# Kernel optimization log

Hardware: AMD Instinct MI355X
Metric: run time of the kernel (lower is better)

The kernel has to match this reference:

```python
import jax, jax.numpy as jnp
import numpy as np

N_LEVELS = 16
N_FEAT = 2
LOG2_T = 19
T = 2 ** LOG2_T
BASE_RES = 2 ** 4
MAX_RES = 2 ** 11
PER_LEVEL_SCALE = np.exp((np.log(MAX_RES) - np.log(BASE_RES)) / (N_LEVELS - 1))
RESOLUTIONS = [int(np.floor(BASE_RES * PER_LEVEL_SCALE ** lv)) + 1 for lv in range(N_LEVELS)]
INIT_ACTIVE_LEVEL = 8
N_POINTS = 1048576
N_OUT = N_LEVELS * N_FEAT
# tcnn spatial hashing primes
P1 = jnp.uint32(2654435761)
P2 = jnp.uint32(805459861)


def _level_lookup(x, tbl, res):
    """x: [N,3] in [0,1], tbl: [T,F], res: python int grid resolution."""
    pos = x * (res - 1)                       # [N,3]
    c0 = jnp.clip(jnp.floor(pos).astype(jnp.int32), 0, res - 2)
    w = pos - c0.astype(pos.dtype)            # [N,3] trilinear fractions
    feats = jnp.zeros((x.shape[0], tbl.shape[-1]), dtype=tbl.dtype)
    dense = (res ** 3) <= T                   # static per level: dense grid vs hashed
    for dz in (0, 1):
        for dy in (0, 1):
            for dx in (0, 1):
                offs = jnp.array([dx, dy, dz], jnp.int32)
                c = c0 + offs                 # [N,3] corner int coords
                if dense:
                    idx = c[:, 0] + res * (c[:, 1] + res * c[:, 2])
                else:
                    cu = c.astype(jnp.uint32)
                    idx = ((cu[:, 0]) ^ (cu[:, 1] * P1) ^ (cu[:, 2] * P2)) & jnp.uint32(T - 1)
                    idx = idx.astype(jnp.int32)
                # trilinear corner weight: prod over axes of (w if offs==1 else 1-w)
                wc = jnp.prod(jnp.where(offs == 1, w, 1.0 - w), axis=-1)  # [N]
                feats = feats + tbl[idx] * wc[:, None]
    return feats


def setup_inputs() -> dict:
    key = jax.random.key(0)
    k1, k2 = jax.random.split(key)
    x = jax.random.uniform(k1, (N_POINTS, 3), dtype=jnp.float32)
    # tcnn-style small uniform init of the hash table
    table = jax.random.uniform(k2, (N_LEVELS, T, N_FEAT), dtype=jnp.float32,
                               minval=-1e-4, maxval=1e-4)
    mask = jnp.concatenate([
        jnp.ones(INIT_ACTIVE_LEVEL * N_FEAT, jnp.float32),
        jnp.zeros((N_LEVELS - INIT_ACTIVE_LEVEL) * N_FEAT, jnp.float32),
    ])
    return {"x": x, "table": table, "mask": mask}


def reference(x, table, mask):
    # multi-resolution hash grid encoding + progressive level mask
    outs = [_level_lookup(x, table[lv], RESOLUTIONS[lv]) for lv in range(N_LEVELS)]
    enc = jnp.concatenate(outs, axis=-1)      # [N, 32]
    return enc * mask
```

## Files before the change

### kernel.cpp

```cpp
#include <hip/hip_runtime.h>
#include <cstdint>
#include <cstddef>


namespace {

constexpr int      kNLevels = 16;
constexpr uint32_t kT       = 1u << 19;
constexpr uint32_t kP1      = 2654435761u;
constexpr uint32_t kP2      = 805459861u;

typedef float v2f __attribute__((ext_vector_type(2)));
typedef float v4f __attribute__((ext_vector_type(4)));

__device__ constexpr int kRes[kNLevels] = {
    17, 23, 31, 43, 59, 81, 112, 154, 213, 295, 407, 562, 777, 1073, 1483, 2049
};

__device__ inline void corner_setup(float px, float py, float pz, int res,
                                    int& cx, int& cy, int& cz,
                                    float& wx, float& wy, float& wz) {
    const float s = (float)(res - 1);
    const float fx = px * s, fy = py * s, fz = pz * s;
    cx = (int)floorf(fx); cy = (int)floorf(fy); cz = (int)floorf(fz);
    cx = min(max(cx, 0), res - 2);
    cy = min(max(cy, 0), res - 2);
    cz = min(max(cz, 0), res - 2);
    wx = fx - (float)cx; wy = fy - (float)cy; wz = fz - (float)cz;
}

__global__ __launch_bounds__(256) void level_kernel(
    const float* __restrict__ x, const float* __restrict__ table,
    const float* __restrict__ mask, float* __restrict__ ws, int n)
{
    const int lv = blockIdx.y;
    const float m0 = mask[2 * lv], m1 = mask[2 * lv + 1];
    if (m0 == 0.0f && m1 == 0.0f) return;

    const int p = blockIdx.x * blockDim.x + threadIdx.x;
    if (p >= n) return;
    const float px = x[3 * p + 0];
    const float py = x[3 * p + 1];
    const float pz = x[3 * p + 2];

    const int res = kRes[lv];
    int cx, cy, cz; float wx, wy, wz;
    corner_setup(px, py, pz, res, cx, cy, cz, wx, wy, wz);
    const float ux = 1.0f - wx, uy = 1.0f - wy, uz = 1.0f - wz;
    const float* __restrict__ tbl = table + (size_t)lv * (size_t)(kT * 2);

    float r0 = 0.0f, r1 = 0.0f;
    if (res <= 80) {
#pragma unroll
        for (int c = 0; c < 4; ++c) {
            const int dy = c & 1, dz = (c >> 1) & 1;
            const uint32_t idx0 =
                (uint32_t)(cx + res * ((cy + dy) + res * (cz + dz)));
            const v2f a = *(const v2f*)(tbl + 2u * idx0);
            const v2f b = *(const v2f*)(tbl + 2u * idx0 + 2);
            const float wyz = (dy ? wy : uy) * (dz ? wz : uz);
            const float w0 = ux * wyz, w1 = wx * wyz;
            r0 = fmaf(a.x, w0, fmaf(b.x, w1, r0));
            r1 = fmaf(a.y, w0, fmaf(b.y, w1, r1));
        }
    } else {
#pragma unroll
        for (int c = 0; c < 8; ++c) {
            const int dx = c & 1, dy = (c >> 1) & 1, dz = (c >> 2) & 1;
            const uint32_t idx =
                (((uint32_t)(cx + dx)) ^ ((uint32_t)(cy + dy) * kP1)
                                       ^ ((uint32_t)(cz + dz) * kP2)) & (kT - 1u);
            const v2f v = *(const v2f*)(tbl + 2u * idx);
            const float w = (dx ? wx : ux) * (dy ? wy : uy) * (dz ? wz : uz);
            r0 = fmaf(v.x, w, r0);
            r1 = fmaf(v.y, w, r1);
        }
    }
    v2f o; o.x = r0; o.y = r1;
    __builtin_nontemporal_store(o, (v2f*)(ws + ((size_t)lv * n + p) * 2));
}

__global__ __launch_bounds__(256) void gather_out_kernel(
    const float* __restrict__ ws, const float* __restrict__ mask,
    float* __restrict__ out, int n)
{
    const int p = blockIdx.x * blockDim.x + threadIdx.x;
    if (p >= n) return;

    v4f o[8];
#pragma unroll
    for (int lv = 0; lv < kNLevels; ++lv) {
        const float m0 = mask[2 * lv], m1 = mask[2 * lv + 1];
        float r0 = 0.0f, r1 = 0.0f;
        if (m0 != 0.0f || m1 != 0.0f) {
            const v2f v = __builtin_nontemporal_load(
                (const v2f*)(ws + ((size_t)lv * n + p) * 2));
            r0 = v.x * m0;
            r1 = v.y * m1;
        }
        if (lv & 1) { o[lv >> 1].z = r0; o[lv >> 1].w = r1; }
        else        { o[lv >> 1].x = r0; o[lv >> 1].y = r1; }
    }
    v4f* __restrict__ op = (v4f*)(out + (size_t)p * 32);
#pragma unroll
    for (int i = 0; i < 8; ++i) op[i] = o[i];
}

__global__ __launch_bounds__(256) void fused_kernel(
    const float* __restrict__ x, const float* __restrict__ table,
    const float* __restrict__ mask, float* __restrict__ out, int n)
{
    const int p = blockIdx.x * blockDim.x + threadIdx.x;
    if (p >= n) return;
    const float px = x[3 * p + 0], py = x[3 * p + 1], pz = x[3 * p + 2];
    v4f o[8];
#pragma unroll
    for (int lv = 0; lv < kNLevels; ++lv) {
        const float m0 = mask[2 * lv], m1 = mask[2 * lv + 1];
        float r0 = 0.0f, r1 = 0.0f;
        if (m0 != 0.0f || m1 != 0.0f) {
            const int res = kRes[lv];
            const bool dense = ((long long)res * res * res) <= (long long)kT;
            int cx, cy, cz; float wx, wy, wz;
            corner_setup(px, py, pz, res, cx, cy, cz, wx, wy, wz);
            const float ux = 1.0f - wx, uy = 1.0f - wy, uz = 1.0f - wz;
            const float* __restrict__ tbl = table + (size_t)lv * (size_t)(kT * 2);
#pragma unroll
            for (int c = 0; c < 8; ++c) {
                const int dx = c & 1, dy = (c >> 1) & 1, dz = (c >> 2) & 1;
                const int ix = cx + dx, iy = cy + dy, iz = cz + dz;
                uint32_t idx;
                if (dense) idx = (uint32_t)(ix + res * (iy + res * iz));
                else idx = (((uint32_t)ix) ^ ((uint32_t)iy * kP1)
                                           ^ ((uint32_t)iz * kP2)) & (kT - 1u);
                const v2f v = *(const v2f*)(tbl + 2u * idx);
                const float w = (dx ? wx : ux) * (dy ? wy : uy) * (dz ? wz : uz);
                r0 = fmaf(v.x, w, r0);
                r1 = fmaf(v.y, w, r1);
            }
            r0 *= m0; r1 *= m1;
        }
        if (lv & 1) { o[lv >> 1].z = r0; o[lv >> 1].w = r1; }
        else        { o[lv >> 1].x = r0; o[lv >> 1].y = r1; }
    }
    v4f* __restrict__ op = (v4f*)(out + (size_t)p * 32);
#pragma unroll
    for (int i = 0; i < 8; ++i) op[i] = o[i];
}

}

extern "C" void kernel_launch(void* const* d_in, const int* in_sizes, int n_in,
                              void* d_out, int out_size, void* d_ws, size_t ws_size,
                              hipStream_t stream) {
    const float* x     = (const float*)d_in[0];
    const float* table = (const float*)d_in[1];
    const float* mask  = (const float*)d_in[2];
    float*       out   = (float*)d_out;

    const int n = in_sizes[0] / 3;
    const int block = 256;
    const int gx = (n + block - 1) / block;

    const size_t ws_needed = (size_t)kNLevels * (size_t)n * 2 * sizeof(float);
    if (ws_size >= ws_needed) {
        float* ws = (float*)d_ws;
        dim3 grid1(gx, kNLevels);
        level_kernel<<<grid1, block, 0, stream>>>(x, table, mask, ws, n);
        gather_out_kernel<<<gx, block, 0, stream>>>(ws, mask, out, n);
    } else {
        fused_kernel<<<gx, block, 0, stream>>>(x, table, mask, out, n);
    }
}
```

Measured before the change: 354.6 us.

## Fuse dense low-resolution levels into the output gather kernel

Levels 0-4 have small dense tables, so they are now computed directly inside the gather/output kernel instead of in the per-level kernel. The per-level kernel now only handles levels 5-15, which shrinks its grid and cuts the workspace write and read traffic by five levels. Dense corner pairs are fetched as a single 16-byte load via memcpy. The cost is that the gather kernel must read x again and do more arithmetic per thread, which may use more registers.

```diff
diff --git a/kernel.cpp b/kernel.cpp
--- a/kernel.cpp
+++ b/kernel.cpp
@@ -29,11 +29,11 @@
     wx = fx - (float)cx; wy = fy - (float)cy; wz = fz - (float)cz;
 }
 
-__global__ __launch_bounds__(256) void level_kernel(
+__global__ __launch_bounds__(256) void hashed_level_kernel(
     const float* __restrict__ x, const float* __restrict__ table,
     const float* __restrict__ mask, float* __restrict__ ws, int n)
 {
-    const int lv = blockIdx.y;
+    const int lv = 5 + blockIdx.y;
     const float m0 = mask[2 * lv], m1 = mask[2 * lv + 1];
     if (m0 == 0.0f && m1 == 0.0f) return;
 
@@ -50,57 +50,77 @@
     const float* __restrict__ tbl = table + (size_t)lv * (size_t)(kT * 2);
 
     float r0 = 0.0f, r1 = 0.0f;
-    if (res <= 80) {
 #pragma unroll
-        for (int c = 0; c < 4; ++c) {
-            const int dy = c & 1, dz = (c >> 1) & 1;
-            const uint32_t idx0 =
-                (uint32_t)(cx + res * ((cy + dy) + res * (cz + dz)));
-            const v2f a = *(const v2f*)(tbl + 2u * idx0);
-            const v2f b = *(const v2f*)(tbl + 2u * idx0 + 2);
-            const float wyz = (dy ? wy : uy) * (dz ? wz : uz);
-            const float w0 = ux * wyz, w1 = wx * wyz;
-            r0 = fmaf(a.x, w0, fmaf(b.x, w1, r0));
-            r1 = fmaf(a.y, w0, fmaf(b.y, w1, r1));
-        }
-    } else {
-#pragma unroll
-        for (int c = 0; c < 8; ++c) {
-            const int dx = c & 1, dy = (c >> 1) & 1, dz = (c >> 2) & 1;
-            const uint32_t idx =
-                (((uint32_t)(cx + dx)) ^ ((uint32_t)(cy + dy) * kP1)
-                                       ^ ((uint32_t)(cz + dz) * kP2)) & (kT - 1u);
-            const v2f v = *(const v2f*)(tbl + 2u * idx);
-            const float w = (dx ? wx : ux) * (dy ? wy : uy) * (dz ? wz : uz);
-            r0 = fmaf(v.x, w, r0);
-            r1 = fmaf(v.y, w, r1);
-        }
+    for (int c = 0; c < 8; ++c) {
+        const int dx = c & 1, dy = (c >> 1) & 1, dz = (c >> 2) & 1;
+        const uint32_t idx =
+            (((uint32_t)(cx + dx)) ^ ((uint32_t)(cy + dy) * kP1)
+                                   ^ ((uint32_t)(cz + dz) * kP2)) & (kT - 1u);
+        const v2f v = *(const v2f*)(tbl + 2u * idx);
+        const float w = (dx ? wx : ux) * (dy ? wy : uy) * (dz ? wz : uz);
+        r0 = fmaf(v.x, w, r0);
+        r1 = fmaf(v.y, w, r1);
     }
     v2f o; o.x = r0; o.y = r1;
-    __builtin_nontemporal_store(o, (v2f*)(ws + ((size_t)lv * n + p) * 2));
+    __builtin_nontemporal_store(
+        o, (v2f*)(ws + ((size_t)(lv - 5) * n + p) * 2));
 }
 
 __global__ __launch_bounds__(256) void gather_out_kernel(
+    const float* __restrict__ x, const float* __restrict__ table,
     const float* __restrict__ ws, const float* __restrict__ mask,
     float* __restrict__ out, int n)
 {
     const int p = blockIdx.x * blockDim.x + threadIdx.x;
     if (p >= n) return;
+    const float px = x[3 * p + 0];
+    const float py = x[3 * p + 1];
+    const float pz = x[3 * p + 2];
 
     v4f o[8];
+
 #pragma unroll
-    for (int lv = 0; lv < kNLevels; ++lv) {
+    for (int lv = 0; lv < 5; ++lv) {
+        const float m0 = mask[2 * lv], m1 = mask[2 * lv + 1];
+        float r0 = 0.0f, r1 = 0.0f;
+        if (m0 != 0.0f || m1 != 0.0f) {
+            const int res = kRes[lv];
+            int cx, cy, cz; float wx, wy, wz;
+            corner_setup(px, py, pz, res, cx, cy, cz, wx, wy, wz);
+            const float ux = 1.0f - wx, uy = 1.0f - wy, uz = 1.0f - wz;
+            const float* __restrict__ tbl = table + (size_t)lv * (size_t)(kT * 2);
+#pragma unroll
+            for (int c = 0; c < 4; ++c) {
+                const int dy = c & 1, dz = (c >> 1) & 1;
+                const uint32_t idx0 =
+                    (uint32_t)(cx + res * ((cy + dy) + res * (cz + dz)));
+                v4f ab;
+                __builtin_memcpy(&ab, tbl + 2u * idx0, sizeof(v4f));
+                const float wyz = (dy ? wy : uy) * (dz ? wz : uz);
+                const float w0 = ux * wyz, w1 = wx * wyz;
+                r0 = fmaf(ab.x, w0, fmaf(ab.z, w1, r0));
+                r1 = fmaf(ab.y, w0, fmaf(ab.w, w1, r1));
+            }
+            r0 *= m0; r1 *= m1;
+        }
+        if (lv & 1) { o[lv >> 1].z = r0; o[lv >> 1].w = r1; }
+        else        { o[lv >> 1].x = r0; o[lv >> 1].y = r1; }
+    }
+
+#pragma unroll
+    for (int lv = 5; lv < kNLevels; ++lv) {
         const float m0 = mask[2 * lv], m1 = mask[2 * lv + 1];
         float r0 = 0.0f, r1 = 0.0f;
         if (m0 != 0.0f || m1 != 0.0f) {
             const v2f v = __builtin_nontemporal_load(
-                (const v2f*)(ws + ((size_t)lv * n + p) * 2));
+                (const v2f*)(ws + ((size_t)(lv - 5) * n + p) * 2));
             r0 = v.x * m0;
             r1 = v.y * m1;
         }
         if (lv & 1) { o[lv >> 1].z = r0; o[lv >> 1].w = r1; }
         else        { o[lv >> 1].x = r0; o[lv >> 1].y = r1; }
     }
+
     v4f* __restrict__ op = (v4f*)(out + (size_t)p * 32);
 #pragma unroll
     for (int i = 0; i < 8; ++i) op[i] = o[i];
@@ -162,12 +182,12 @@
     const int block = 256;
     const int gx = (n + block - 1) / block;
 
-    const size_t ws_needed = (size_t)kNLevels * (size_t)n * 2 * sizeof(float);
+    const size_t ws_needed = (size_t)(kNLevels - 5) * (size_t)n * 2 * sizeof(float);
     if (ws_size >= ws_needed) {
         float* ws = (float*)d_ws;
-        dim3 grid1(gx, kNLevels);
-        level_kernel<<<grid1, block, 0, stream>>>(x, table, mask, ws, n);
-        gather_out_kernel<<<gx, block, 0, stream>>>(ws, mask, out, n);
+        dim3 grid1(gx, kNLevels - 5);
+        hashed_level_kernel<<<grid1, block, 0, stream>>>(x, table, mask, ws, n);
+        gather_out_kernel<<<gx, block, 0, stream>>>(x, table, ws, mask, out, n);
     } else {
         fused_kernel<<<gx, block, 0, stream>>>(x, table, mask, out, n);
     }
```

Measured after the change: 350.7 us. About the same (-1.1%).
